# Kernel optimization log

Measured on AMD Instinct MI355X. Metric: run time of the kernel, lower is better.

## Reference

```python
import jax, jax.numpy as jnp
import numpy as np
from jax import lax

B, S, I, H, O, L = 64, 512, 512, 1024, 512, 2


def setup_inputs() -> dict:
    key = jax.random.key(0)
    ks = jax.random.split(key, 12)
    s_ih0 = 1.0 / np.sqrt(H)
    inp = {
        "x": jax.random.normal(ks[0], (B, S, I), dtype=jnp.float32),
        # PyTorch LSTM params: weight_ih_l{k} [4H, in], weight_hh_l{k} [4H, H], biases [4H]
        "W_ih0": jax.random.uniform(ks[1], (4 * H, I), minval=-s_ih0, maxval=s_ih0),
        "W_hh0": jax.random.uniform(ks[2], (4 * H, H), minval=-s_ih0, maxval=s_ih0),
        "b_ih0": jax.random.uniform(ks[3], (4 * H,), minval=-s_ih0, maxval=s_ih0),
        "b_hh0": jax.random.uniform(ks[4], (4 * H,), minval=-s_ih0, maxval=s_ih0),
        "W_ih1": jax.random.uniform(ks[5], (4 * H, H), minval=-s_ih0, maxval=s_ih0),
        "W_hh1": jax.random.uniform(ks[6], (4 * H, H), minval=-s_ih0, maxval=s_ih0),
        "b_ih1": jax.random.uniform(ks[7], (4 * H,), minval=-s_ih0, maxval=s_ih0),
        "b_hh1": jax.random.uniform(ks[8], (4 * H,), minval=-s_ih0, maxval=s_ih0),
        "W_fc": jax.random.uniform(ks[9], (O, H), minval=-s_ih0, maxval=s_ih0),
        "b_fc": jax.random.uniform(ks[10], (O,), minval=-s_ih0, maxval=s_ih0),
    }
    return inp


def lstm_layer(x, W_ih, W_hh, b_ih, b_hh):
    # x: [B, S, in]; zero initial h/c (module's init_hidden). Gate order i,f,g,o (PyTorch).
    b, s = x.shape[0], x.shape[1]
    h0 = jnp.zeros((b, H), dtype=x.dtype)
    c0 = jnp.zeros((b, H), dtype=x.dtype)
    # Precompute input contribution for all timesteps: [S, B, 4H]
    xg = jnp.einsum('bsi,gi->sbg', x, W_ih) + b_ih + b_hh

    def step(carry, xg_t):
        h, c = carry
        g = xg_t + h @ W_hh.T  # [B, 4H]
        i, f, gg, o = jnp.split(g, 4, axis=-1)
        i = jax.nn.sigmoid(i)
        f = jax.nn.sigmoid(f)
        gg = jnp.tanh(gg)
        o = jax.nn.sigmoid(o)
        c = f * c + i * gg
        h = o * jnp.tanh(c)
        return (h, c), h

    (h_n, c_n), ys = lax.scan(step, (h0, c0), xg)
    return jnp.swapaxes(ys, 0, 1), h_n, c_n  # [B, S, H]


def reference(x, W_ih0, W_hh0, b_ih0, b_hh0, W_ih1, W_hh1, b_ih1, b_hh1, W_fc, b_fc):
    y0, h0n, c0n = lstm_layer(x, W_ih0, W_hh0, b_ih0, b_hh0)
    y1, h1n, c1n = lstm_layer(y0, W_ih1, W_hh1, b_ih1, b_hh1)
    h_n = jnp.stack([h0n, h1n], axis=0)  # [L, B, H]
    c_n = jnp.stack([c0n, c1n], axis=0)
    out = y1.reshape(-1, H) @ W_fc.T + b_fc  # [B*S, O]
    return out, h_n, c_n
```

## Files before the change

### kernel.cpp

```cpp
#include <hip/hip_runtime.h>
#include <hip/hip_bf16.h>

#define B_   64
#define S_   512
#define I_   512
#define H_   1024
#define G4H  4096
#define O_   512
#define CH_  32
#define NCH  (S_ / CH_)

#define NBLK   128
#define THR_   512
#define LSTR   8
#define BARSTR 32

typedef short s16x8 __attribute__((ext_vector_type(8)));
typedef short s16x4 __attribute__((ext_vector_type(4)));
typedef float f32x4 __attribute__((ext_vector_type(4)));
typedef unsigned long long u64;
using bf16 = __hip_bfloat16;

__device__ __forceinline__ float bf2f(bf16 v) { return __bfloat162float(v); }
__device__ __forceinline__ bf16  f2bf(float f) { return __float2bfloat16(f); }
__device__ __forceinline__ short f2bfb(float f) { bf16 h = __float2bfloat16(f); return *(short*)&h; }

__device__ __forceinline__ void storeC(float* p, float v) { *p = v; }
__device__ __forceinline__ void storeC(bf16* p, float v)  { *p = f2bf(v); }

template <int AMAP, int CMAP, int ABF, typename CT>
__global__ __launch_bounds__(256) void gemm_bt(
    const void* __restrict__ Av, const float* __restrict__ Bw,
    CT* __restrict__ C,
    const float* __restrict__ bias1, const float* __restrict__ bias2,
    int M, int N, int K, int t0)
{
    __shared__ bf16 As[128 * 40];
    __shared__ bf16 Bs[128 * 40];

    const int tid  = threadIdx.x;
    const int wave = tid >> 6;
    const int lane = tid & 63;
    const int quad = lane >> 4;
    const int l16  = lane & 15;

    const int m_base = blockIdx.x * 128;
    const int n_base = blockIdx.y * 128;
    const int wm = (wave >> 1) * 64;
    const int wn = (wave & 1) * 64;

    f32x4 acc[4][4] = {};

    for (int k0 = 0; k0 < K; k0 += 32) {
        __syncthreads();
#pragma unroll
        for (int i = 0; i < 2; i++) {
            int l   = tid + i * 256;
            int row = l >> 2;
            int ko  = (l & 3) * 8;
            int m   = m_base + row;
            long ar = m;
            if (AMAP == 1) ar = (long)(m & 63) * S_ + t0 + (m >> 6);

            if (ABF) {
                const bf16* ap = (const bf16*)Av + ar * (long)K + k0 + ko;
                *(s16x8*)(&As[row * 40 + ko]) = *(const s16x8*)ap;
            } else {
                const float* ap = (const float*)Av + ar * (long)K + k0 + ko;
                f32x4 a0 = *(const f32x4*)ap;
                f32x4 a1 = *(const f32x4*)(ap + 4);
                s16x8 av;
#pragma unroll
                for (int j = 0; j < 4; j++) { av[j] = f2bfb(a0[j]); av[4 + j] = f2bfb(a1[j]); }
                *(s16x8*)(&As[row * 40 + ko]) = av;
            }

            const float* bp = &Bw[(long)(n_base + row) * K + k0 + ko];
            f32x4 b0 = *(const f32x4*)bp;
            f32x4 b1 = *(const f32x4*)(bp + 4);
            s16x8 bv;
#pragma unroll
            for (int j = 0; j < 4; j++) { bv[j] = f2bfb(b0[j]); bv[4 + j] = f2bfb(b1[j]); }
            *(s16x8*)(&Bs[row * 40 + ko]) = bv;
        }
        __syncthreads();

        s16x8 af[4], bfr[4];
#pragma unroll
        for (int i = 0; i < 4; i++)
            af[i] = *(const s16x8*)(&As[(wm + i * 16 + l16) * 40 + quad * 8]);
#pragma unroll
        for (int j = 0; j < 4; j++)
            bfr[j] = *(const s16x8*)(&Bs[(wn + j * 16 + l16) * 40 + quad * 8]);
#pragma unroll
        for (int i = 0; i < 4; i++)
#pragma unroll
            for (int j = 0; j < 4; j++)
                acc[i][j] = __builtin_amdgcn_mfma_f32_16x16x32_bf16(af[i], bfr[j], acc[i][j], 0, 0, 0);
    }

#pragma unroll
    for (int i = 0; i < 4; i++) {
#pragma unroll
        for (int j = 0; j < 4; j++) {
#pragma unroll
            for (int r = 0; r < 4; r++) {
                int m = m_base + wm + i * 16 + quad * 4 + r;
                int n = n_base + wn + j * 16 + l16;
                float v = acc[i][j][r];
                if (bias1) v += bias1[n];
                if (bias2) v += bias2[n];
                long cr = m;
                if (CMAP == 2) cr = (long)(m & 63) * S_ + t0 + (m >> 6);
                storeC(&C[cr * (long)N + n], v);
            }
        }
    }
}

__device__ __forceinline__ void grid_bar(unsigned* ctr, unsigned target)
{
    __syncthreads();
    const int t = threadIdx.x;
    if (t == 0)
        __hip_atomic_fetch_add(ctr + ((blockIdx.x & 63) & (LSTR - 1)) * BARSTR, 1u,
                               __ATOMIC_RELAXED, __HIP_MEMORY_SCOPE_AGENT);
    if (t < LSTR) {
        while (__hip_atomic_load(ctr + t * BARSTR, __ATOMIC_RELAXED,
                                 __HIP_MEMORY_SCOPE_AGENT) < target)
            __builtin_amdgcn_s_sleep(1);
    }
    __syncthreads();
}

__global__ __launch_bounds__(THR_, 1) void chunk_k(
    const bf16* __restrict__ xg0,
    const bf16* __restrict__ xg1,
    const float* __restrict__ Whh0,
    const float* __restrict__ Whh1,
    bf16* __restrict__ h0w,
    bf16* __restrict__ h1w,
    float* __restrict__ c0,
    float* __restrict__ c1,
    unsigned* __restrict__ bar,
    int cpar, int do0, int do1)
{
    const int layer  = blockIdx.x >> 6;
    const int nb     = blockIdx.x & 63;
    const int active = layer ? do1 : do0;
    if (!active) return;

    const bf16*  xg  = layer ? xg1  : xg0;
    const float* Whh = layer ? Whh1 : Whh0;
    float*       cst = layer ? c1   : c0;

    bf16 *rbuf, *cbuf;
    if (layer == 0) {
        rbuf = h0w + (size_t)(cpar & 1) * (CH_ + 1) * B_ * H_;
        cbuf = h0w + (size_t)((cpar + 1) & 1) * (CH_ + 1) * B_ * H_;
    } else {
        rbuf = h1w; cbuf = h1w;
    }

    const int tid  = threadIdx.x;
    const int lane = tid & 63;
    const int wave = tid >> 6;
    const int quad = lane >> 4;
    const int l16  = lane & 15;
    const int kw   = wave >> 2;
    const int mw   = wave & 3;

    unsigned* barL = bar + (size_t)layer * CH_ * LSTR * BARSTR;
    const unsigned bar_tgt =
        (layer ? (unsigned)cpar : (unsigned)(cpar + 1)) * (64 / LSTR);

    __shared__ bf16  wsh[64][1032];
    __shared__ float gs[64][68];

    {
        int r  = tid >> 3;
        int cc = (tid & 7) * 128;
        const float* src = Whh + ((long)(r >> 4) * H_ + nb * 16 + (r & 15)) * H_ + cc;
#pragma unroll
        for (int q = 0; q < 128; q += 4) {
            f32x4 v = *(const f32x4*)(src + q);
            s16x4 o;
#pragma unroll
            for (int w = 0; w < 4; w++) o[w] = f2bfb(v[w]);
            *(s16x4*)(&wsh[r][cc + q]) = o;
        }
    }
    __syncthreads();

    const int uu   = tid & 15;
    const int unit = nb * 16 + uu;
    float creg[2];
#pragma unroll
    for (int rep = 0; rep < 2; rep++) {
        int bb = (tid + rep * 512) >> 4;
        creg[rep] = cst[(long)bb * H_ + unit];
    }

    float xn[2][4];
#pragma unroll
    for (int rep = 0; rep < 2; rep++) {
        int bb = (tid + rep * 512) >> 4;
#pragma unroll
        for (int g = 0; g < 4; g++)
            xn[rep][g] = bf2f(xg[(long)bb * G4H + (long)g * H_ + unit]);
    }

    for (int j = 0; j < CH_; j++) {
        const u64* ap = (const u64*)(rbuf + (long)j * (B_ * H_)
                       + (long)(mw * 16 + l16) * H_ + kw * 512) + quad * 2;
        u64 la[16], lb[16];
#pragma unroll
        for (int t = 0; t < 16; t++) {
            u64* p = (u64*)(ap + (size_t)t * 8);
            la[t] = __hip_atomic_load(p,     __ATOMIC_RELAXED, __HIP_MEMORY_SCOPE_AGENT);
            lb[t] = __hip_atomic_load(p + 1, __ATOMIC_RELAXED, __HIP_MEMORY_SCOPE_AGENT);
        }

        f32x4 acc[4] = {};
#pragma unroll
        for (int t = 0; t < 16; t++) {
            union { u64 q[2]; s16x8 v; } ua;
            ua.q[0] = la[t]; ua.q[1] = lb[t];
            int k = kw * 512 + t * 32;
#pragma unroll
            for (int cf = 0; cf < 4; cf++) {
                s16x8 b = *(const s16x8*)(&wsh[cf * 16 + l16][k + quad * 8]);
                acc[cf] = __builtin_amdgcn_mfma_f32_16x16x32_bf16(ua.v, b, acc[cf], 0, 0, 0);
            }
        }

        if (kw == 0) {
#pragma unroll
            for (int cf = 0; cf < 4; cf++)
#pragma unroll
                for (int r = 0; r < 4; r++)
                    gs[mw * 16 + quad * 4 + r][cf * 16 + l16] = acc[cf][r];
        }
        __syncthreads();
        if (kw == 1) {
#pragma unroll
            for (int cf = 0; cf < 4; cf++)
#pragma unroll
                for (int r = 0; r < 4; r++)
                    gs[mw * 16 + quad * 4 + r][cf * 16 + l16] += acc[cf][r];
        }
        __syncthreads();

        unsigned short hb[2];
#pragma unroll
        for (int rep = 0; rep < 2; rep++) {
            int bb = (tid + rep * 512) >> 4;
            float gi = gs[bb][uu]      + xn[rep][0];
            float gf = gs[bb][16 + uu] + xn[rep][1];
            float gg = gs[bb][32 + uu] + xn[rep][2];
            float go = gs[bb][48 + uu] + xn[rep][3];

            float ig = 1.f / (1.f + __expf(-gi));
            float fg = 1.f / (1.f + __expf(-gf));
            float og = 1.f / (1.f + __expf(-go));
            float e2 = __expf(-2.f * fabsf(gg));
            float tg = (1.f - e2) / (1.f + e2);
            tg = (gg < 0.f) ? -tg : tg;

            creg[rep] = fg * creg[rep] + ig * tg;
            float e2c = __expf(-2.f * fabsf(creg[rep]));
            float tc = (1.f - e2c) / (1.f + e2c);
            tc = (creg[rep] < 0.f) ? -tc : tc;

            bf16 hv = f2bf(og * tc);
            hb[rep] = *(unsigned short*)&hv;
        }
#pragma unroll
        for (int rep = 0; rep < 2; rep++) {
            int bb = (tid + rep * 512) >> 4;
            unsigned my    = hb[rep];
            unsigned other = (unsigned)__shfl((int)my, lane ^ 1, 64);
            if (!(uu & 1)) {
                unsigned v32 = my | (other << 16);
                unsigned* dst = (unsigned*)(rbuf + (long)(j + 1) * (B_ * H_)
                                + (long)bb * H_ + unit);
                __hip_atomic_store(dst, v32, __ATOMIC_RELAXED, __HIP_MEMORY_SCOPE_AGENT);
                if (j == CH_ - 1) {
                    unsigned* cd = (unsigned*)(cbuf + (long)bb * H_ + unit);
                    __hip_atomic_store(cd, v32, __ATOMIC_RELAXED, __HIP_MEMORY_SCOPE_AGENT);
                }
            }
        }

        if (j + 1 < CH_) {
            const bf16* xq = xg + (long)(j + 1) * (B_ * G4H);
#pragma unroll
            for (int rep = 0; rep < 2; rep++) {
                int bb = (tid + rep * 512) >> 4;
#pragma unroll
                for (int g = 0; g < 4; g++)
                    xn[rep][g] = bf2f(xq[(long)bb * G4H + (long)g * H_ + unit]);
            }
        }

        if (j < CH_ - 1)
            grid_bar(barL + (size_t)j * LSTR * BARSTR, bar_tgt);
    }

#pragma unroll
    for (int rep = 0; rep < 2; rep++) {
        int bb = (tid + rep * 512) >> 4;
        cst[(long)bb * H_ + unit] = creg[rep];
    }
}

__global__ __launch_bounds__(256) void init_k(
    float* c0, float* c1, bf16* h0w, bf16* h1w, unsigned* bar, int nbar)
{
    int i = blockIdx.x * 256 + threadIdx.x;
    if (i < B_ * H_) {
        c0[i] = 0.f; c1[i] = 0.f;
        h0w[i] = f2bf(0.f);
        h1w[i] = f2bf(0.f);
    }
    if (i < nbar) bar[i] = 0u;
}

__global__ __launch_bounds__(256) void finalize_k(
    const bf16* __restrict__ h0w, const bf16* __restrict__ h1w,
    const float* __restrict__ c0, const float* __restrict__ c1,
    float* __restrict__ out_hn, float* __restrict__ out_cn)
{
    int i = blockIdx.x * 256 + threadIdx.x;
    if (i < B_ * H_) {
        out_hn[i]            = bf2f(h0w[i]);
        out_hn[B_ * H_ + i]  = bf2f(h1w[i]);
        out_cn[i]            = c0[i];
        out_cn[B_ * H_ + i]  = c1[i];
    }
}

extern "C" void kernel_launch(void* const* d_in, const int* in_sizes, int n_in,
                              void* d_out, int out_size, void* d_ws, size_t ws_size,
                              hipStream_t stream)
{
    const float* x    = (const float*)d_in[0];
    const float* Wih0 = (const float*)d_in[1];
    const float* Whh0 = (const float*)d_in[2];
    const float* bih0 = (const float*)d_in[3];
    const float* bhh0 = (const float*)d_in[4];
    const float* Wih1 = (const float*)d_in[5];
    const float* Whh1 = (const float*)d_in[6];
    const float* bih1 = (const float*)d_in[7];
    const float* bhh1 = (const float*)d_in[8];
    const float* Wfc  = (const float*)d_in[9];
    const float* bfc  = (const float*)d_in[10];
    float* out = (float*)d_out;

    char* p = (char*)d_ws;
    float* c0  = (float*)p; p += (size_t)B_ * H_ * 4;
    float* c1  = (float*)p; p += (size_t)B_ * H_ * 4;
    bf16* h0w  = (bf16*)p;  p += (size_t)2 * (CH_ + 1) * B_ * H_ * 2;
    bf16* h1w  = (bf16*)p;  p += (size_t)(CH_ + 1) * B_ * H_ * 2;
    bf16* xg0  = (bf16*)p;  p += (size_t)CH_ * B_ * G4H * 2;
    bf16* xg1  = (bf16*)p;  p += (size_t)CH_ * B_ * G4H * 2;
    unsigned* bar = (unsigned*)p;
    const int nbar = 2 * CH_ * LSTR * BARSTR;
    p += (size_t)nbar * 4;

    init_k<<<(B_ * H_ + 255) / 256, 256, 0, stream>>>(c0, c1, h0w, h1w, bar, nbar);

    const dim3 gxg0((B_ * CH_) / 128, G4H / 128);
    const dim3 gfc((B_ * CH_) / 128, O_ / 128);

    for (int c = 0; c <= NCH; c++) {
        const int do0 = (c < NCH);
        const int do1 = (c >= 1);

        if (do0) {
            gemm_bt<1, 0, 0, bf16><<<gxg0, 256, 0, stream>>>(
                x, Wih0, xg0, bih0, bhh0, B_ * CH_, G4H, I_, c * CH_);
        }
        if (do1) {
            const bf16* h0chunk = h0w + (size_t)((c - 1) & 1) * (CH_ + 1) * B_ * H_ + B_ * H_;
            gemm_bt<0, 0, 1, bf16><<<gxg0, 256, 0, stream>>>(
                h0chunk, Wih1, xg1, bih1, bhh1, B_ * CH_, G4H, H_, 0);
        }

        {
            const bf16*  a0  = xg0;  const bf16*  a1  = xg1;
            const float* w0  = Whh0; const float* w1  = Whh1;
            bf16* hp0 = h0w; bf16* hp1 = h1w;
            float* cp0 = c0; float* cp1 = c1;
            unsigned* bp = bar;
            int cv = c, d0 = do0, d1 = do1;
            void* args[] = { &a0, &a1, &w0, &w1, &hp0, &hp1,
                             &cp0, &cp1, &bp, &cv, &d0, &d1 };
            hipLaunchCooperativeKernel((const void*)chunk_k,
                                       dim3(NBLK), dim3(THR_), args, 0, stream);
        }

        if (do1) {
            gemm_bt<0, 2, 1, float><<<gfc, 256, 0, stream>>>(
                h1w + B_ * H_, Wfc, out, bfc, (const float*)nullptr,
                B_ * CH_, O_, H_, (c - 1) * CH_);
        }
    }

    finalize_k<<<(B_ * H_ + 255) / 256, 256, 0, stream>>>(
        h0w, h1w, c0, c1,
        out + (size_t)B_ * S_ * O_,
        out + (size_t)B_ * S_ * O_ + 2 * (size_t)B_ * H_);
}
```

Measured before the change: 8.125 ms.

## Replace grid barrier with per-batch-group counters and drop K-split reduction

Removes the global grid barrier between recurrent timesteps. Each wave now bumps a counter for the batch rows it produced after draining its stores, and each consumer wave waits only on the two counters covering its own 16 batch rows before reading h. The wave decomposition also moves from a K-split (two waves per output tile, added through shared memory with an extra syncthreads) to each wave covering the full K for two gate column tiles, which removes the accumulate pass but doubles the per-wave register load buffer. Correctness relies on relaxed atomics plus a vmcnt wait to order the h stores before the counter increment.

After: 12.64 ms. 1.56x slower.

```diff
diff --git a/kernel.cpp b/kernel.cpp
--- a/kernel.cpp
+++ b/kernel.cpp
@@ -12,7 +12,7 @@
 
 #define NBLK   128
 #define THR_   512
-#define LSTR   8
+#define NGRP   8
 #define BARSTR 32
 
 typedef short s16x8 __attribute__((ext_vector_type(8)));
@@ -116,21 +116,6 @@
             }
         }
     }
-}
-
-__device__ __forceinline__ void grid_bar(unsigned* ctr, unsigned target)
-{
-    __syncthreads();
-    const int t = threadIdx.x;
-    if (t == 0)
-        __hip_atomic_fetch_add(ctr + ((blockIdx.x & 63) & (LSTR - 1)) * BARSTR, 1u,
-                               __ATOMIC_RELAXED, __HIP_MEMORY_SCOPE_AGENT);
-    if (t < LSTR) {
-        while (__hip_atomic_load(ctr + t * BARSTR, __ATOMIC_RELAXED,
-                                 __HIP_MEMORY_SCOPE_AGENT) < target)
-            __builtin_amdgcn_s_sleep(1);
-    }
-    __syncthreads();
 }
 
 __global__ __launch_bounds__(THR_, 1) void chunk_k(
@@ -167,12 +152,11 @@
     const int wave = tid >> 6;
     const int quad = lane >> 4;
     const int l16  = lane & 15;
-    const int kw   = wave >> 2;
-    const int mw   = wave & 3;
-
-    unsigned* barL = bar + (size_t)layer * CH_ * LSTR * BARSTR;
-    const unsigned bar_tgt =
-        (layer ? (unsigned)cpar : (unsigned)(cpar + 1)) * (64 / LSTR);
+    const int cw   = wave & 1;
+    const int mw   = wave >> 1;
+
+    unsigned* barL = bar + (size_t)layer * (CH_ - 1) * NGRP * BARSTR;
+    const unsigned bar_tgt = (layer ? (unsigned)cpar : (unsigned)(cpar + 1)) * 128u;
 
     __shared__ bf16  wsh[64][1032];
     __shared__ float gs[64][68];
@@ -211,47 +195,48 @@
     }
 
     for (int j = 0; j < CH_; j++) {
+        if (j > 0) {
+            unsigned* cj = barL + (size_t)(j - 1) * NGRP * BARSTR;
+            while (__hip_atomic_load(cj + (2 * mw) * BARSTR, __ATOMIC_RELAXED,
+                                     __HIP_MEMORY_SCOPE_AGENT) < bar_tgt)
+                __builtin_amdgcn_s_sleep(1);
+            while (__hip_atomic_load(cj + (2 * mw + 1) * BARSTR, __ATOMIC_RELAXED,
+                                     __HIP_MEMORY_SCOPE_AGENT) < bar_tgt)
+                __builtin_amdgcn_s_sleep(1);
+            __builtin_amdgcn_sched_barrier(0);
+            asm volatile("" ::: "memory");
+        }
+
         const u64* ap = (const u64*)(rbuf + (long)j * (B_ * H_)
-                       + (long)(mw * 16 + l16) * H_ + kw * 512) + quad * 2;
-        u64 la[16], lb[16];
-#pragma unroll
-        for (int t = 0; t < 16; t++) {
+                       + (long)(mw * 16 + l16) * H_) + quad * 2;
+        u64 la[32], lb[32];
+#pragma unroll
+        for (int t = 0; t < 32; t++) {
             u64* p = (u64*)(ap + (size_t)t * 8);
             la[t] = __hip_atomic_load(p,     __ATOMIC_RELAXED, __HIP_MEMORY_SCOPE_AGENT);
             lb[t] = __hip_atomic_load(p + 1, __ATOMIC_RELAXED, __HIP_MEMORY_SCOPE_AGENT);
         }
 
-        f32x4 acc[4] = {};
-#pragma unroll
-        for (int t = 0; t < 16; t++) {
+        f32x4 acc0 = {}, acc1 = {};
+#pragma unroll
+        for (int t = 0; t < 32; t++) {
             union { u64 q[2]; s16x8 v; } ua;
             ua.q[0] = la[t]; ua.q[1] = lb[t];
-            int k = kw * 512 + t * 32;
-#pragma unroll
-            for (int cf = 0; cf < 4; cf++) {
-                s16x8 b = *(const s16x8*)(&wsh[cf * 16 + l16][k + quad * 8]);
-                acc[cf] = __builtin_amdgcn_mfma_f32_16x16x32_bf16(ua.v, b, acc[cf], 0, 0, 0);
-            }
-        }
-
-        if (kw == 0) {
-#pragma unroll
-            for (int cf = 0; cf < 4; cf++)
-#pragma unroll
-                for (int r = 0; r < 4; r++)
-                    gs[mw * 16 + quad * 4 + r][cf * 16 + l16] = acc[cf][r];
+            int k = t * 32;
+            s16x8 b0 = *(const s16x8*)(&wsh[(2 * cw + 0) * 16 + l16][k + quad * 8]);
+            s16x8 b1 = *(const s16x8*)(&wsh[(2 * cw + 1) * 16 + l16][k + quad * 8]);
+            acc0 = __builtin_amdgcn_mfma_f32_16x16x32_bf16(ua.v, b0, acc0, 0, 0, 0);
+            acc1 = __builtin_amdgcn_mfma_f32_16x16x32_bf16(ua.v, b1, acc1, 0, 0, 0);
+        }
+
+#pragma unroll
+        for (int r = 0; r < 4; r++) {
+            int m = mw * 16 + quad * 4 + r;
+            gs[m][(2 * cw + 0) * 16 + l16] = acc0[r];
+            gs[m][(2 * cw + 1) * 16 + l16] = acc1[r];
         }
         __syncthreads();
-        if (kw == 1) {
-#pragma unroll
-            for (int cf = 0; cf < 4; cf++)
-#pragma unroll
-                for (int r = 0; r < 4; r++)
-                    gs[mw * 16 + quad * 4 + r][cf * 16 + l16] += acc[cf][r];
-        }
-        __syncthreads();
-
-        unsigned short hb[2];
+
 #pragma unroll
         for (int rep = 0; rep < 2; rep++) {
             int bb = (tid + rep * 512) >> 4;
@@ -273,12 +258,7 @@
             tc = (creg[rep] < 0.f) ? -tc : tc;
 
             bf16 hv = f2bf(og * tc);
-            hb[rep] = *(unsigned short*)&hv;
-        }
-#pragma unroll
-        for (int rep = 0; rep < 2; rep++) {
-            int bb = (tid + rep * 512) >> 4;
-            unsigned my    = hb[rep];
+            unsigned my    = *(unsigned short*)&hv;
             unsigned other = (unsigned)__shfl((int)my, lane ^ 1, 64);
             if (!(uu & 1)) {
                 unsigned v32 = my | (other << 16);
@@ -290,6 +270,11 @@
                     __hip_atomic_store(cd, v32, __ATOMIC_RELAXED, __HIP_MEMORY_SCOPE_AGENT);
                 }
             }
+            asm volatile("s_waitcnt vmcnt(0)" ::: "memory");
+            if (j < CH_ - 1 && lane == 0)
+                __hip_atomic_fetch_add(
+                    barL + ((size_t)j * NGRP + rep * 4 + (wave >> 1)) * BARSTR, 1u,
+                    __ATOMIC_RELAXED, __HIP_MEMORY_SCOPE_AGENT);
         }
 
         if (j + 1 < CH_) {
@@ -303,8 +288,7 @@
             }
         }
 
-        if (j < CH_ - 1)
-            grid_bar(barL + (size_t)j * LSTR * BARSTR, bar_tgt);
+        __syncthreads();
     }
 
 #pragma unroll
@@ -365,7 +349,7 @@
     bf16* xg0  = (bf16*)p;  p += (size_t)CH_ * B_ * G4H * 2;
     bf16* xg1  = (bf16*)p;  p += (size_t)CH_ * B_ * G4H * 2;
     unsigned* bar = (unsigned*)p;
-    const int nbar = 2 * CH_ * LSTR * BARSTR;
+    const int nbar = 2 * (CH_ - 1) * NGRP * BARSTR;
     p += (size_t)nbar * 4;
 
     init_k<<<(B_ * H_ + 255) / 256, 256, 0, stream>>>(c0, c1, h0w, h1w, bar, nbar);
```

## Fuse input-projection and FC GEMMs into cooperative recurrence kernel as pipelined side blocks

Applied to the files above, without the earlier changes.

Replaces the per-chunk sequence of separate GEMM launches plus the cooperative recurrence kernel with one cooperative kernel of 256 blocks. The first 128 blocks run the two layers' recurrences. The other 128 blocks compute the next chunk's layer-0 input projection, the layer-1 projection of the previous chunk's h0, and the FC output of an older chunk. Chunk size is halved, and the xg and h buffers are double-buffered so the stages run skewed across chunks. The aim is to hide GEMM work behind the latency-bound recurrence and cut launch counts. In exchange the chunk count and grid barrier count double, and the GEMM blocks share the device with the recurrence blocks.

Measured after the change: 6.683 ms. -17.8%, faster.

```diff
diff --git a/kernel.cpp b/kernel.cpp
--- a/kernel.cpp
+++ b/kernel.cpp
@@ -7,13 +7,13 @@
 #define H_   1024
 #define G4H  4096
 #define O_   512
-#define CH_  32
+#define CH_  16
 #define NCH  (S_ / CH_)
 
-#define NBLK   128
-#define THR_   512
 #define LSTR   8
 #define BARSTR 32
+#define HWSZ   ((CH_ + 1) * B_ * H_)
+#define XGSZ   (CH_ * B_ * G4H)
 
 typedef short s16x8 __attribute__((ext_vector_type(8)));
 typedef short s16x4 __attribute__((ext_vector_type(4)));
@@ -100,9 +100,9 @@
     }
 
 #pragma unroll
-    for (int i = 0; i < 4; i++) {
-#pragma unroll
-        for (int j = 0; j < 4; j++) {
+    for (int i = 0; i < 4; i++)
+#pragma unroll
+        for (int j = 0; j < 4; j++)
 #pragma unroll
             for (int r = 0; r < 4; r++) {
                 int m = m_base + wm + i * 16 + quad * 4 + r;
@@ -114,8 +114,90 @@
                 if (CMAP == 2) cr = (long)(m & 63) * S_ + t0 + (m >> 6);
                 storeC(&C[cr * (long)N + n], v);
             }
-        }
-    }
+}
+
+__device__ void gemm_tile(const void* Av, const float* Bw, void* Cv,
+                          const float* bias1, const float* bias2,
+                          int N, int K, int t0, int amap, int cmap,
+                          int abf, int cbf, int tx, int ty, char* smem)
+{
+    bf16* As = (bf16*)smem;
+    bf16* Bs = (bf16*)(smem + 128 * 40 * 2);
+
+    const int tid  = threadIdx.x;
+    const int wave = tid >> 6;
+    const int lane = tid & 63;
+    const int quad = lane >> 4;
+    const int l16  = lane & 15;
+    const int m_base = tx * 128;
+    const int n_base = ty * 128;
+    const int wm = (wave >> 2) * 64;
+    const int wn = (wave & 3) * 32;
+
+    f32x4 acc[4][2] = {};
+
+    for (int k0 = 0; k0 < K; k0 += 32) {
+        __syncthreads();
+        {
+            int l   = tid;
+            int row = l >> 2;
+            int ko  = (l & 3) * 8;
+            int m   = m_base + row;
+            long ar = m;
+            if (amap == 1) ar = (long)(m & 63) * S_ + t0 + (m >> 6);
+
+            if (abf) {
+                const bf16* ap = (const bf16*)Av + ar * (long)K + k0 + ko;
+                *(s16x8*)(&As[row * 40 + ko]) = *(const s16x8*)ap;
+            } else {
+                const float* ap = (const float*)Av + ar * (long)K + k0 + ko;
+                f32x4 a0 = *(const f32x4*)ap;
+                f32x4 a1 = *(const f32x4*)(ap + 4);
+                s16x8 av;
+#pragma unroll
+                for (int j = 0; j < 4; j++) { av[j] = f2bfb(a0[j]); av[4 + j] = f2bfb(a1[j]); }
+                *(s16x8*)(&As[row * 40 + ko]) = av;
+            }
+            const float* bp = &Bw[(long)(n_base + row) * K + k0 + ko];
+            f32x4 b0 = *(const f32x4*)bp;
+            f32x4 b1 = *(const f32x4*)(bp + 4);
+            s16x8 bv;
+#pragma unroll
+            for (int j = 0; j < 4; j++) { bv[j] = f2bfb(b0[j]); bv[4 + j] = f2bfb(b1[j]); }
+            *(s16x8*)(&Bs[row * 40 + ko]) = bv;
+        }
+        __syncthreads();
+
+        s16x8 af[4], bfr[2];
+#pragma unroll
+        for (int i = 0; i < 4; i++)
+            af[i] = *(const s16x8*)(&As[(wm + i * 16 + l16) * 40 + quad * 8]);
+#pragma unroll
+        for (int j = 0; j < 2; j++)
+            bfr[j] = *(const s16x8*)(&Bs[(wn + j * 16 + l16) * 40 + quad * 8]);
+#pragma unroll
+        for (int i = 0; i < 4; i++)
+#pragma unroll
+            for (int j = 0; j < 2; j++)
+                acc[i][j] = __builtin_amdgcn_mfma_f32_16x16x32_bf16(af[i], bfr[j], acc[i][j], 0, 0, 0);
+    }
+
+#pragma unroll
+    for (int i = 0; i < 4; i++)
+#pragma unroll
+        for (int j = 0; j < 2; j++)
+#pragma unroll
+            for (int r = 0; r < 4; r++) {
+                int m = m_base + wm + i * 16 + quad * 4 + r;
+                int n = n_base + wn + j * 16 + l16;
+                float v = acc[i][j][r];
+                if (bias1) v += bias1[n];
+                if (bias2) v += bias2[n];
+                long cr = m;
+                if (cmap == 2) cr = (long)(m & 63) * S_ + t0 + (m >> 6);
+                if (cbf) storeC((bf16*)Cv + cr * (long)N + n, v);
+                else     storeC((float*)Cv + cr * (long)N + n, v);
+            }
 }
 
 __device__ __forceinline__ void grid_bar(unsigned* ctr, unsigned target)
@@ -133,34 +215,63 @@
     __syncthreads();
 }
 
-__global__ __launch_bounds__(THR_, 1) void chunk_k(
-    const bf16* __restrict__ xg0,
-    const bf16* __restrict__ xg1,
-    const float* __restrict__ Whh0,
-    const float* __restrict__ Whh1,
-    bf16* __restrict__ h0w,
-    bf16* __restrict__ h1w,
-    float* __restrict__ c0,
-    float* __restrict__ c1,
-    unsigned* __restrict__ bar,
-    int cpar, int do0, int do1)
-{
+__global__ __launch_bounds__(512, 1) void fused_k(
+    const float* __restrict__ x,
+    const float* __restrict__ Wih0, const float* __restrict__ Wih1,
+    const float* __restrict__ Wfc,
+    const float* __restrict__ bih0, const float* __restrict__ bhh0,
+    const float* __restrict__ bih1, const float* __restrict__ bhh1,
+    const float* __restrict__ bfc,
+    const float* __restrict__ Whh0, const float* __restrict__ Whh1,
+    bf16* __restrict__ h0w, bf16* __restrict__ h1w,
+    bf16* __restrict__ xg0, bf16* __restrict__ xg1,
+    float* __restrict__ c0, float* __restrict__ c1,
+    float* __restrict__ out,
+    unsigned* __restrict__ bar, int cpar, int do0, int do1)
+{
+    __shared__ __align__(16) char smem[149504];
+
+    if (blockIdx.x >= 128) {
+        const int a = blockIdx.x - 128;
+        const int n_xg0 = (cpar <= NCH - 2) ? 256 : 0;
+        const int n_xg1 = (cpar >= 1 && cpar <= NCH) ? 256 : 0;
+        const int n_fc  = (cpar >= 3) ? 32 : 0;
+        const int ntot  = n_xg0 + n_xg1 + n_fc;
+        for (int idx = a; idx < ntot; idx += 128) {
+            if (idx < n_xg0) {
+                int tx = idx & 7, ty = idx >> 3;
+                gemm_tile(x, Wih0, xg0 + (size_t)((cpar + 1) & 1) * XGSZ,
+                          bih0, bhh0, G4H, I_, (cpar + 1) * CH_,
+                          1, 0, 0, 1, tx, ty, smem);
+            } else if (idx < n_xg0 + n_xg1) {
+                int k = idx - n_xg0, tx = k & 7, ty = k >> 3;
+                gemm_tile(h0w + (size_t)((cpar - 1) & 1) * HWSZ + B_ * H_, Wih1,
+                          xg1 + (size_t)((cpar - 1) & 1) * XGSZ,
+                          bih1, bhh1, G4H, H_, 0,
+                          0, 0, 1, 1, tx, ty, smem);
+            } else {
+                int k = idx - n_xg0 - n_xg1, tx = k & 7, ty = k >> 3;
+                gemm_tile(h1w + (size_t)((cpar - 3) & 1) * HWSZ + B_ * H_, Wfc,
+                          out, bfc, (const float*)nullptr, O_, H_, (cpar - 3) * CH_,
+                          0, 2, 1, 0, tx, ty, smem);
+            }
+        }
+        return;
+    }
+
     const int layer  = blockIdx.x >> 6;
     const int nb     = blockIdx.x & 63;
     const int active = layer ? do1 : do0;
     if (!active) return;
 
-    const bf16*  xg  = layer ? xg1  : xg0;
+    const bf16*  xg  = layer ? (xg1 + (size_t)(cpar & 1) * XGSZ)
+                             : (xg0 + (size_t)(cpar & 1) * XGSZ);
     const float* Whh = layer ? Whh1 : Whh0;
     float*       cst = layer ? c1   : c0;
 
-    bf16 *rbuf, *cbuf;
-    if (layer == 0) {
-        rbuf = h0w + (size_t)(cpar & 1) * (CH_ + 1) * B_ * H_;
-        cbuf = h0w + (size_t)((cpar + 1) & 1) * (CH_ + 1) * B_ * H_;
-    } else {
-        rbuf = h1w; cbuf = h1w;
-    }
+    bf16* hwb = layer ? h1w : h0w;
+    bf16* rbuf = hwb + (size_t)(cpar & 1) * HWSZ;
+    bf16* cbuf = hwb + (size_t)((cpar + 1) & 1) * HWSZ;
 
     const int tid  = threadIdx.x;
     const int lane = tid & 63;
@@ -170,12 +281,12 @@
     const int kw   = wave >> 2;
     const int mw   = wave & 3;
 
-    unsigned* barL = bar + (size_t)layer * CH_ * LSTR * BARSTR;
+    unsigned* barL = bar + (size_t)layer * (CH_ - 1) * LSTR * BARSTR;
     const unsigned bar_tgt =
-        (layer ? (unsigned)cpar : (unsigned)(cpar + 1)) * (64 / LSTR);
-
-    __shared__ bf16  wsh[64][1032];
-    __shared__ float gs[64][68];
+        (layer ? (unsigned)(cpar - 1) : (unsigned)(cpar + 1)) * (64 / LSTR);
+
+    bf16*  wsh = (bf16*)smem;
+    float* gs  = (float*)(smem + 132096);
 
     {
         int r  = tid >> 3;
@@ -187,7 +298,7 @@
             s16x4 o;
 #pragma unroll
             for (int w = 0; w < 4; w++) o[w] = f2bfb(v[w]);
-            *(s16x4*)(&wsh[r][cc + q]) = o;
+            *(s16x4*)(&wsh[r * 1032 + cc + q]) = o;
         }
     }
     __syncthreads();
@@ -229,7 +340,7 @@
             int k = kw * 512 + t * 32;
 #pragma unroll
             for (int cf = 0; cf < 4; cf++) {
-                s16x8 b = *(const s16x8*)(&wsh[cf * 16 + l16][k + quad * 8]);
+                s16x8 b = *(const s16x8*)(&wsh[(cf * 16 + l16) * 1032 + k + quad * 8]);
                 acc[cf] = __builtin_amdgcn_mfma_f32_16x16x32_bf16(ua.v, b, acc[cf], 0, 0, 0);
             }
         }
@@ -239,7 +350,7 @@
             for (int cf = 0; cf < 4; cf++)
 #pragma unroll
                 for (int r = 0; r < 4; r++)
-                    gs[mw * 16 + quad * 4 + r][cf * 16 + l16] = acc[cf][r];
+                    gs[(mw * 16 + quad * 4 + r) * 68 + cf * 16 + l16] = acc[cf][r];
         }
         __syncthreads();
         if (kw == 1) {
@@ -247,7 +358,7 @@
             for (int cf = 0; cf < 4; cf++)
 #pragma unroll
                 for (int r = 0; r < 4; r++)
-                    gs[mw * 16 + quad * 4 + r][cf * 16 + l16] += acc[cf][r];
+                    gs[(mw * 16 + quad * 4 + r) * 68 + cf * 16 + l16] += acc[cf][r];
         }
         __syncthreads();
 
@@ -255,10 +366,10 @@
 #pragma unroll
         for (int rep = 0; rep < 2; rep++) {
             int bb = (tid + rep * 512) >> 4;
-            float gi = gs[bb][uu]      + xn[rep][0];
-            float gf = gs[bb][16 + uu] + xn[rep][1];
-            float gg = gs[bb][32 + uu] + xn[rep][2];
-            float go = gs[bb][48 + uu] + xn[rep][3];
+            float gi = gs[bb * 68 + uu]      + xn[rep][0];
+            float gf = gs[bb * 68 + 16 + uu] + xn[rep][1];
+            float gg = gs[bb * 68 + 32 + uu] + xn[rep][2];
+            float go = gs[bb * 68 + 48 + uu] + xn[rep][3];
 
             float ig = 1.f / (1.f + __expf(-gi));
             float fg = 1.f / (1.f + __expf(-gf));
@@ -360,51 +471,45 @@
     char* p = (char*)d_ws;
     float* c0  = (float*)p; p += (size_t)B_ * H_ * 4;
     float* c1  = (float*)p; p += (size_t)B_ * H_ * 4;
-    bf16* h0w  = (bf16*)p;  p += (size_t)2 * (CH_ + 1) * B_ * H_ * 2;
-    bf16* h1w  = (bf16*)p;  p += (size_t)(CH_ + 1) * B_ * H_ * 2;
-    bf16* xg0  = (bf16*)p;  p += (size_t)CH_ * B_ * G4H * 2;
-    bf16* xg1  = (bf16*)p;  p += (size_t)CH_ * B_ * G4H * 2;
+    bf16* h0w  = (bf16*)p;  p += (size_t)2 * HWSZ * 2;
+    bf16* h1w  = (bf16*)p;  p += (size_t)2 * HWSZ * 2;
+    bf16* xg0  = (bf16*)p;  p += (size_t)2 * XGSZ * 2;
+    bf16* xg1  = (bf16*)p;  p += (size_t)2 * XGSZ * 2;
     unsigned* bar = (unsigned*)p;
-    const int nbar = 2 * CH_ * LSTR * BARSTR;
+    const int nbar = 2 * (CH_ - 1) * LSTR * BARSTR;
     p += (size_t)nbar * 4;
 
     init_k<<<(B_ * H_ + 255) / 256, 256, 0, stream>>>(c0, c1, h0w, h1w, bar, nbar);
 
-    const dim3 gxg0((B_ * CH_) / 128, G4H / 128);
-    const dim3 gfc((B_ * CH_) / 128, O_ / 128);
-
-    for (int c = 0; c <= NCH; c++) {
-        const int do0 = (c < NCH);
-        const int do1 = (c >= 1);
-
-        if (do0) {
-            gemm_bt<1, 0, 0, bf16><<<gxg0, 256, 0, stream>>>(
-                x, Wih0, xg0, bih0, bhh0, B_ * CH_, G4H, I_, c * CH_);
-        }
-        if (do1) {
-            const bf16* h0chunk = h0w + (size_t)((c - 1) & 1) * (CH_ + 1) * B_ * H_ + B_ * H_;
-            gemm_bt<0, 0, 1, bf16><<<gxg0, 256, 0, stream>>>(
-                h0chunk, Wih1, xg1, bih1, bhh1, B_ * CH_, G4H, H_, 0);
-        }
-
-        {
-            const bf16*  a0  = xg0;  const bf16*  a1  = xg1;
-            const float* w0  = Whh0; const float* w1  = Whh1;
-            bf16* hp0 = h0w; bf16* hp1 = h1w;
-            float* cp0 = c0; float* cp1 = c1;
-            unsigned* bp = bar;
-            int cv = c, d0 = do0, d1 = do1;
-            void* args[] = { &a0, &a1, &w0, &w1, &hp0, &hp1,
-                             &cp0, &cp1, &bp, &cv, &d0, &d1 };
-            hipLaunchCooperativeKernel((const void*)chunk_k,
-                                       dim3(NBLK), dim3(THR_), args, 0, stream);
-        }
-
-        if (do1) {
-            gemm_bt<0, 2, 1, float><<<gfc, 256, 0, stream>>>(
-                h1w + B_ * H_, Wfc, out, bfc, (const float*)nullptr,
-                B_ * CH_, O_, H_, (c - 1) * CH_);
-        }
+    {
+        dim3 g((B_ * CH_) / 128, G4H / 128);
+        gemm_bt<1, 0, 0, bf16><<<g, 256, 0, stream>>>(
+            x, Wih0, xg0, bih0, bhh0, B_ * CH_, G4H, I_, 0);
+    }
+
+    for (int c = 0; c <= NCH + 1; c++) {
+        int d0 = (c <= NCH - 1);
+        int d1 = (c >= 2);
+        const float* xa = x;
+        const float* wi0 = Wih0; const float* wi1 = Wih1; const float* wfc = Wfc;
+        const float* b0i = bih0; const float* b0h = bhh0;
+        const float* b1i = bih1; const float* b1h = bhh1; const float* bf_ = bfc;
+        const float* wh0 = Whh0; const float* wh1 = Whh1;
+        bf16* hp0 = h0w; bf16* hp1 = h1w; bf16* xp0 = xg0; bf16* xp1 = xg1;
+        float* cp0 = c0; float* cp1 = c1; float* op = out;
+        unsigned* bp = bar; int cv = c;
+        void* args[] = { &xa, &wi0, &wi1, &wfc, &b0i, &b0h, &b1i, &b1h, &bf_,
+                         &wh0, &wh1, &hp0, &hp1, &xp0, &xp1, &cp0, &cp1, &op,
+                         &bp, &cv, &d0, &d1 };
+        hipLaunchCooperativeKernel((const void*)fused_k,
+                                   dim3(256), dim3(512), args, 0, stream);
+    }
+
+    {
+        dim3 g((B_ * CH_) / 128, O_ / 128);
+        gemm_bt<0, 2, 1, float><<<g, 256, 0, stream>>>(
+            h1w + (size_t)((NCH - 1) & 1) * HWSZ + B_ * H_, Wfc, out, bfc,
+            (const float*)nullptr, B_ * CH_, O_, H_, (NCH - 1) * CH_);
     }
 
     finalize_k<<<(B_ * H_ + 255) / 256, 256, 0, stream>>>(
```
